# Performance work log

Hardware: AMD Instinct MI355X
Metric: run time of the kernel (lower is better)

The kernel has to match this reference:

```python
import jax, jax.numpy as jnp
import numpy as np

D2, D1, T1, T2, D3, T3 = 120, 40, 10, 5, 3, 1


def _kaiming_uniform(key, shape):
    # torch kaiming_uniform_ with nonlinearity='relu': bound = sqrt(6/fan_in), fan_in = shape[1]
    bound = np.sqrt(6.0 / shape[1])
    return jax.random.uniform(key, shape, jnp.float32, -bound, bound)


def setup_inputs() -> dict:
    key = jax.random.key(0)
    ks = jax.random.split(key, 6)
    x = jax.random.normal(ks[0], (131072, D1, T1), jnp.float32)
    return {
        "x": x,
        "BL_W1": _kaiming_uniform(ks[1], (D2, D1)),
        "BL_W2": _kaiming_uniform(ks[2], (T1, T2)),
        "BL_B": jnp.zeros((D2, T2), jnp.float32),
        "T_W1": _kaiming_uniform(ks[3], (D3, D2)),
        "T_W": jnp.full((T2, T2), 1.0 / T2, jnp.float32),
        "T_W2": _kaiming_uniform(ks[4], (T2, T3)),
        "T_B": jnp.zeros((D3, T3), jnp.float32),
        "l": jnp.full((1,), 0.5, jnp.float32),
    }


def _max_norm(w):
    # torch max_norm_: if frobenius norm > 10, rescale to norm 10 (done under no_grad)
    n = jnp.linalg.norm(w)
    scale = jnp.where(n > 10.0, 10.0 / (1e-8 + n), 1.0)
    return w * jax.lax.stop_gradient(scale)


def reference(x, BL_W1, BL_W2, BL_B, T_W1, T_W, T_W2, T_B, l):
    # --- weight clamps performed at the top of m_btabl.forward ---
    W1a = _max_norm(BL_W1)
    W2a = _max_norm(BL_W2)
    W1b = _max_norm(T_W1)
    Wb = _max_norm(T_W)
    W2b = _max_norm(T_W2)
    lam = jnp.clip(l[0], 0.0, 1.0)  # l.data clamped to [0,1]

    # BL layer: relu(W1 @ x @ W2 + B); x: [B, D1, T1] -> [B, D2, T2]
    h = jax.nn.relu(jnp.einsum('ed,bdt->bet', W1a, x) @ W2a + BL_B)
    # dropout(0.1) is identity at inference

    # TABL layer (t1 here = T2 = 5)
    X = jnp.einsum('ed,bdt->bet', W1b, h)          # [B, D3, T2]
    eye = jnp.eye(T2, dtype=jnp.float32)
    Wm = Wb - Wb * eye + eye / T2                  # force diagonal to 1/t1
    A = jax.nn.softmax(X @ Wm, axis=-1)            # temporal attention
    X = lam * X + (1.0 - lam) * X * A              # convex combination
    y = X @ W2b + T_B                              # [B, D3, 1]

    y = jnp.squeeze(y)                             # [B, D3]
    return jax.nn.softmax(y, axis=1)
```

## Files before the change

### kernel.cpp

```cpp
#include <hip/hip_runtime.h>


typedef float f32x16 __attribute__((ext_vector_type(16)));
typedef float f32x8  __attribute__((ext_vector_type(8)));
typedef float f32x4t __attribute__((ext_vector_type(4)));

#define NT 256

__device__ __forceinline__ float block_reduce_sum(float v, float* red, int tid) {
    #pragma unroll
    for (int off = 32; off > 0; off >>= 1) v += __shfl_xor(v, off, 64);
    if ((tid & 63) == 0) red[tid >> 6] = v;
    __syncthreads();
    float r = red[0] + red[1] + red[2] + red[3];
    __syncthreads();
    return r;
}

__global__ __launch_bounds__(NT)
void prep_kernel(const float* __restrict__ W1, const float* __restrict__ W2,
                 const float* __restrict__ B,  const float* __restrict__ Tw1,
                 const float* __restrict__ Tw, const float* __restrict__ Tw2,
                 const float* __restrict__ TB, const float* __restrict__ l,
                 float* __restrict__ ws)
{
    __shared__ float red[4];
    const int tid = threadIdx.x;
    float ss;
    ss = 0.f; for (int i = tid; i < 4800; i += NT) { float w = W1[i];  ss += w*w; }
    const float n1 = sqrtf(block_reduce_sum(ss, red, tid));
    ss = 0.f; for (int i = tid; i < 50;   i += NT) { float w = W2[i];  ss += w*w; }
    const float n2 = sqrtf(block_reduce_sum(ss, red, tid));
    ss = 0.f; for (int i = tid; i < 360;  i += NT) { float w = Tw1[i]; ss += w*w; }
    const float n3 = sqrtf(block_reduce_sum(ss, red, tid));
    ss = 0.f; for (int i = tid; i < 25;   i += NT) { float w = Tw[i];  ss += w*w; }
    const float n4 = sqrtf(block_reduce_sum(ss, red, tid));
    ss = 0.f; for (int i = tid; i < 5;    i += NT) { float w = Tw2[i]; ss += w*w; }
    const float n5 = sqrtf(block_reduce_sum(ss, red, tid));

    const float s1 = n1 > 10.f ? 10.f/(1e-8f+n1) : 1.f;
    const float s2 = n2 > 10.f ? 10.f/(1e-8f+n2) : 1.f;
    const float s3 = n3 > 10.f ? 10.f/(1e-8f+n3) : 1.f;
    const float s4 = n4 > 10.f ? 10.f/(1e-8f+n4) : 1.f;
    const float s5 = n5 > 10.f ? 10.f/(1e-8f+n5) : 1.f;

    for (int i = tid; i < 4800; i += NT) { int e = i/40,  d = i - e*40;  ws[e*48+d]      = W1[i]*s1; }
    for (int i = tid; i < 600;  i += NT) { int e = i/5,   t = i - e*5;   ws[e*48+40+t]   = B[i];     }
    for (int i = tid; i < 360;  i += NT) { int j = i/120, e = i - j*120; ws[e*48+45+j]   = Tw1[i]*s3;}
    for (int i = tid; i < 48;   i += NT) ws[120*48 + i] = 0.f;
    for (int i = tid; i < 52;   i += NT) ws[5824 + i] = (i < 50) ? W2[i]*s2 : 0.f;
    for (int i = tid; i < 36;   i += NT) {
        float v = 0.f;
        if (i < 25)      { int r = i/5, c = i - r*5; v = (r==c) ? 0.2f : Tw[i]*s4; }
        else if (i < 30) v = Tw2[i-25]*s5;
        else if (i < 33) v = TB[i-30];
        else if (i == 33){ float lv = l[0]; v = fminf(fmaxf(lv, 0.f), 1.f); }
        ws[5888 + i] = v;
    }
}

__device__ __forceinline__ float pair_sum(float v) {
    int o = __builtin_amdgcn_update_dpp(0, __float_as_int(v), 0xB1, 0xF, 0xF, true);
    return v + __int_as_float(o);
}

__device__ __forceinline__ float w2f(const f32x16& a, const f32x16& b,
                                     const f32x16& c, const f32x4t& d, int i) {
    return i < 16 ? a[i] : i < 32 ? b[i-16] : i < 48 ? c[i-32] : d[i-48];
}
__device__ __forceinline__ float c3f(const f32x16& a, const f32x16& b,
                                     const f32x4t& c, int i) {
    return i < 16 ? a[i] : i < 32 ? b[i-16] : c[i-32];
}

__global__ __launch_bounds__(NT, 3)
void btabl_main(const float* __restrict__ x, const float* __restrict__ ws,
                float* __restrict__ out, int nsamp)
{
    __shared__ float sRec[5808];

    const int tid = threadIdx.x;
    {
        const float4* src = (const float4*)ws;
        float4* dst = (float4*)sRec;
        for (int i = tid; i < 1452; i += NT) dst[i] = src[i];
    }
    __syncthreads();

    f32x16 wa, wb, wc; f32x4t wd;
    {
        const float* w2p = ws + 5824;
        asm volatile("s_load_dwordx16 %0, %4, 0x0\n\t"
                     "s_load_dwordx16 %1, %4, 0x40\n\t"
                     "s_load_dwordx16 %2, %4, 0x80\n\t"
                     "s_load_dwordx4  %3, %4, 0xc0\n\t"
                     "s_waitcnt lgkmcnt(0)"
                     : "=&s"(wa), "=&s"(wb), "=&s"(wc), "=&s"(wd)
                     : "s"(w2p));
    }

    const int pair = tid >> 1;
    const int p    = tid & 1;
    const int s    = blockIdx.x * 128 + pair;
    if (s >= nsamp) return;

    const float* xs = x + (size_t)s*400 + p*200;

    float Z[20][5];
    #pragma unroll
    for (int d0 = 0; d0 < 20; d0 += 2) {
        const float4* xv = (const float4*)(xs + d0*10);
        float4 f0 = xv[0], f1 = xv[1], f2 = xv[2], f3 = xv[3], f4 = xv[4];
        float v[20] = {f0.x,f0.y,f0.z,f0.w, f1.x,f1.y,f1.z,f1.w,
                       f2.x,f2.y,f2.z,f2.w, f3.x,f3.y,f3.z,f3.w,
                       f4.x,f4.y,f4.z,f4.w};
        #pragma unroll
        for (int r = 0; r < 2; r++) {
            #pragma unroll
            for (int t = 0; t < 5; t++) {
                float a = 0.f;
                #pragma unroll
                for (int k = 0; k < 10; k++)
                    a = fmaf(v[r*10+k], w2f(wa,wb,wc,wd, k*5+t), a);
                Z[d0+r][t] = a;
            }
        }
    }

    f32x8 bw;
    {
        const float* bp = ws + 40;
        asm volatile("s_load_dwordx8 %0, %1, 0x0\n\ts_waitcnt lgkmcnt(0)"
                     : "=&s"(bw) : "s"(bp));
    }
    float X3[15];
    #pragma unroll
    for (int i = 0; i < 15; i++) X3[i] = 0.f;

    for (int e = 0; e < 120; e++) {
        f32x8 bwn;
        {
            const float* bpn = ws + (e+1)*48 + 40;
            asm volatile("s_load_dwordx8 %0, %1, 0x0" : "=&s"(bwn) : "s"(bpn));
        }

        const float4* wr = (const float4*)(&sRec[e*48 + p*20]);
        float acc[5] = {0.f,0.f,0.f,0.f,0.f};
        #pragma unroll
        for (int c = 0; c < 5; c++) {
            float4 w = wr[c];
            #pragma unroll
            for (int t = 0; t < 5; t++) {
                acc[t] = fmaf(w.x, Z[c*4+0][t], acc[t]);
                acc[t] = fmaf(w.y, Z[c*4+1][t], acc[t]);
                acc[t] = fmaf(w.z, Z[c*4+2][t], acc[t]);
                acc[t] = fmaf(w.w, Z[c*4+3][t], acc[t]);
            }
        }
        #pragma unroll
        for (int t = 0; t < 5; t++) acc[t] = pair_sum(acc[t]);

        #pragma unroll
        for (int t = 0; t < 5; t++) {
            float h = fmaxf(acc[t] + bw[t], 0.f);
            X3[t]    = fmaf(bw[5], h, X3[t]);
            X3[5+t]  = fmaf(bw[6], h, X3[5+t]);
            X3[10+t] = fmaf(bw[7], h, X3[10+t]);
        }

        asm volatile("s_waitcnt lgkmcnt(0)" : "+s"(bwn));
        bw = bwn;
    }

    f32x16 ca, cb; f32x4t cc;
    {
        const float* cp = ws + 5888;
        asm volatile("s_load_dwordx16 %0, %3, 0x0\n\t"
                     "s_load_dwordx16 %1, %3, 0x40\n\t"
                     "s_load_dwordx4  %2, %3, 0x80\n\t"
                     "s_waitcnt lgkmcnt(0)"
                     : "=&s"(ca), "=&s"(cb), "=&s"(cc)
                     : "s"(cp));
    }
    const float lam  = c3f(ca, cb, cc, 33);
    const float olam = 1.f - lam;

    float y[3];
    #pragma unroll
    for (int j = 0; j < 3; j++) {
        float Sr[5];
        #pragma unroll
        for (int t = 0; t < 5; t++) {
            float a = 0.f;
            #pragma unroll
            for (int k = 0; k < 5; k++)
                a = fmaf(X3[j*5+k], c3f(ca, cb, cc, k*5+t), a);
            Sr[t] = a;
        }
        float m = Sr[0];
        #pragma unroll
        for (int t = 1; t < 5; t++) m = fmaxf(m, Sr[t]);
        float ex[5], se = 0.f;
        #pragma unroll
        for (int t = 0; t < 5; t++) { ex[t] = __expf(Sr[t]-m); se += ex[t]; }
        const float inv = 1.f/se;
        float yj = c3f(ca, cb, cc, 30+j);
        #pragma unroll
        for (int t = 0; t < 5; t++) {
            float a  = ex[t]*inv;
            float xc = X3[j*5+t]*(lam + olam*a);
            yj = fmaf(xc, c3f(ca, cb, cc, 25+t), yj);
        }
        y[j] = yj;
    }
    float m  = fmaxf(y[0], fmaxf(y[1], y[2]));
    float e0 = __expf(y[0]-m), e1 = __expf(y[1]-m), e2 = __expf(y[2]-m);
    float inv = 1.f/(e0+e1+e2);
    if (p == 0) {
        float* o = out + (size_t)s*3;
        o[0] = e0*inv; o[1] = e1*inv; o[2] = e2*inv;
    }
}

extern "C" void kernel_launch(void* const* d_in, const int* in_sizes, int n_in,
                              void* d_out, int out_size, void* d_ws, size_t ws_size,
                              hipStream_t stream) {
    const float* x   = (const float*)d_in[0];
    const float* W1  = (const float*)d_in[1];
    const float* W2  = (const float*)d_in[2];
    const float* B   = (const float*)d_in[3];
    const float* Tw1 = (const float*)d_in[4];
    const float* Tw  = (const float*)d_in[5];
    const float* Tw2 = (const float*)d_in[6];
    const float* TB  = (const float*)d_in[7];
    const float* l   = (const float*)d_in[8];
    float* out = (float*)d_out;
    float* ws  = (float*)d_ws;

    hipLaunchKernelGGL(prep_kernel, dim3(1), dim3(NT), 0, stream,
                       W1, W2, B, Tw1, Tw, Tw2, TB, l, ws);

    const int nsamp = in_sizes[0] / 400;
    const int grid  = (nsamp + 127) / 128;
    hipLaunchKernelGGL(btabl_main, dim3(grid), dim3(NT), 0, stream,
                       x, ws, out, nsamp);
}
```

Before: 410.3 us.

## Move the D1-to-D2 contraction onto bf16 MFMA with shared-memory staging

The 120x40 W1 contraction, previously done with per-thread fp32 FMAs, now runs as bf16 MFMA 16x16x32 tiles. W1 and the bias are packed into a bf16 image, and the bias is folded in through a one-hot column appended to Z. Each block handles 64 samples with 320 threads: five threads per sample compute the W2 projection and write bf16 Z into LDS, the waves run the MFMAs and reduce into X3, and one wave finishes the attention and softmax. This aims to remove the VALU-bound inner loop, but it gives up accuracy by rounding x·W2 and W1 to bf16, and it adds LDS traffic and two block barriers.

```diff
diff --git a/kernel.cpp b/kernel.cpp
--- a/kernel.cpp
+++ b/kernel.cpp
@@ -1,11 +1,17 @@
 #include <hip/hip_runtime.h>
 
 
-typedef float f32x16 __attribute__((ext_vector_type(16)));
-typedef float f32x8  __attribute__((ext_vector_type(8)));
-typedef float f32x4t __attribute__((ext_vector_type(4)));
-
-#define NT 256
+typedef short bf16x8 __attribute__((ext_vector_type(8)));
+typedef float f32x4v __attribute__((ext_vector_type(4)));
+
+#define NTP 256
+#define NTM 320
+
+__device__ __forceinline__ unsigned short f2bf(float f) {
+    unsigned int u = __float_as_uint(f);
+    u += 0x7FFFu + ((u >> 16) & 1u);
+    return (unsigned short)(u >> 16);
+}
 
 __device__ __forceinline__ float block_reduce_sum(float v, float* red, int tid) {
     #pragma unroll
@@ -17,7 +23,7 @@
     return r;
 }
 
-__global__ __launch_bounds__(NT)
+__global__ __launch_bounds__(NTP)
 void prep_kernel(const float* __restrict__ W1, const float* __restrict__ W2,
                  const float* __restrict__ B,  const float* __restrict__ Tw1,
                  const float* __restrict__ Tw, const float* __restrict__ Tw2,
@@ -27,15 +33,15 @@
     __shared__ float red[4];
     const int tid = threadIdx.x;
     float ss;
-    ss = 0.f; for (int i = tid; i < 4800; i += NT) { float w = W1[i];  ss += w*w; }
+    ss = 0.f; for (int i = tid; i < 4800; i += NTP) { float w = W1[i];  ss += w*w; }
     const float n1 = sqrtf(block_reduce_sum(ss, red, tid));
-    ss = 0.f; for (int i = tid; i < 50;   i += NT) { float w = W2[i];  ss += w*w; }
+    ss = 0.f; for (int i = tid; i < 50;   i += NTP) { float w = W2[i];  ss += w*w; }
     const float n2 = sqrtf(block_reduce_sum(ss, red, tid));
-    ss = 0.f; for (int i = tid; i < 360;  i += NT) { float w = Tw1[i]; ss += w*w; }
+    ss = 0.f; for (int i = tid; i < 360;  i += NTP) { float w = Tw1[i]; ss += w*w; }
     const float n3 = sqrtf(block_reduce_sum(ss, red, tid));
-    ss = 0.f; for (int i = tid; i < 25;   i += NT) { float w = Tw[i];  ss += w*w; }
+    ss = 0.f; for (int i = tid; i < 25;   i += NTP) { float w = Tw[i];  ss += w*w; }
     const float n4 = sqrtf(block_reduce_sum(ss, red, tid));
-    ss = 0.f; for (int i = tid; i < 5;    i += NT) { float w = Tw2[i]; ss += w*w; }
+    ss = 0.f; for (int i = tid; i < 5;    i += NTP) { float w = Tw2[i]; ss += w*w; }
     const float n5 = sqrtf(block_reduce_sum(ss, red, tid));
 
     const float s1 = n1 > 10.f ? 10.f/(1e-8f+n1) : 1.f;
@@ -44,181 +50,208 @@
     const float s4 = n4 > 10.f ? 10.f/(1e-8f+n4) : 1.f;
     const float s5 = n5 > 10.f ? 10.f/(1e-8f+n5) : 1.f;
 
-    for (int i = tid; i < 4800; i += NT) { int e = i/40,  d = i - e*40;  ws[e*48+d]      = W1[i]*s1; }
-    for (int i = tid; i < 600;  i += NT) { int e = i/5,   t = i - e*5;   ws[e*48+40+t]   = B[i];     }
-    for (int i = tid; i < 360;  i += NT) { int j = i/120, e = i - j*120; ws[e*48+45+j]   = Tw1[i]*s3;}
-    for (int i = tid; i < 48;   i += NT) ws[120*48 + i] = 0.f;
-    for (int i = tid; i < 52;   i += NT) ws[5824 + i] = (i < 50) ? W2[i]*s2 : 0.f;
-    for (int i = tid; i < 36;   i += NT) {
+    unsigned short* img = (unsigned short*)ws;
+    for (int i = tid; i < 129*48; i += NTP) {
+        const int e = i / 48, k = i - e*48;
         float v = 0.f;
-        if (i < 25)      { int r = i/5, c = i - r*5; v = (r==c) ? 0.2f : Tw[i]*s4; }
-        else if (i < 30) v = Tw2[i-25]*s5;
+        if (e < 120) {
+            if (k < 40)      v = W1[e*40 + k] * s1;
+            else if (k < 45) v = B[e*5 + (k-40)];
+        }
+        img[i] = f2bf(v);
+    }
+    for (int i = tid; i < 512; i += NTP) {
+        const int e = i >> 2, c = i & 3;
+        ws[3096 + i] = (c < 3 && e < 120) ? Tw1[c*120 + e] * s3 : 0.f;
+    }
+    for (int i = tid; i < 36; i += NTP) {
+        float v = 0.f;
+        if (i < 25)      { int r = i/5, c = i - r*5; v = (r == c) ? 0.2f : Tw[i]*s4; }
+        else if (i < 30) v = Tw2[i-25] * s5;
         else if (i < 33) v = TB[i-30];
         else if (i == 33){ float lv = l[0]; v = fminf(fmaxf(lv, 0.f), 1.f); }
-        ws[5888 + i] = v;
-    }
-}
-
-__device__ __forceinline__ float pair_sum(float v) {
-    int o = __builtin_amdgcn_update_dpp(0, __float_as_int(v), 0xB1, 0xF, 0xF, true);
-    return v + __int_as_float(o);
-}
-
-__device__ __forceinline__ float w2f(const f32x16& a, const f32x16& b,
-                                     const f32x16& c, const f32x4t& d, int i) {
-    return i < 16 ? a[i] : i < 32 ? b[i-16] : i < 48 ? c[i-32] : d[i-48];
-}
-__device__ __forceinline__ float c3f(const f32x16& a, const f32x16& b,
-                                     const f32x4t& c, int i) {
-    return i < 16 ? a[i] : i < 32 ? b[i-16] : c[i-32];
-}
-
-__global__ __launch_bounds__(NT, 3)
+        ws[3608 + i] = v;
+    }
+    for (int i = tid; i < 50; i += NTP) ws[3644 + i] = W2[i] * s2;
+}
+
+__global__ __launch_bounds__(NTM)
 void btabl_main(const float* __restrict__ x, const float* __restrict__ ws,
                 float* __restrict__ out, int nsamp)
 {
-    __shared__ float sRec[5808];
+    __align__(16) __shared__ unsigned short sW1[129*48];
+    __align__(16) __shared__ float          sWp[128*4];
+    __align__(16) __shared__ float          sC[36];
+    __align__(16) __shared__ unsigned short sZ[320*48 + 16];
+    __align__(16) __shared__ float          sX3[320*3];
 
     const int tid = threadIdx.x;
+
     {
         const float4* src = (const float4*)ws;
-        float4* dst = (float4*)sRec;
-        for (int i = tid; i < 1452; i += NT) dst[i] = src[i];
-    }
-    __syncthreads();
-
-    f32x16 wa, wb, wc; f32x4t wd;
+        float4* d1 = (float4*)sW1;
+        for (int i = tid; i < 774; i += NTM) d1[i] = src[i];
+        float4* d2 = (float4*)sWp;
+        for (int i = tid; i < 128; i += NTM) d2[i] = src[774 + i];
+        if (tid < 9) ((float4*)sC)[tid] = src[902 + tid];
+    }
+
     {
-        const float* w2p = ws + 5824;
-        asm volatile("s_load_dwordx16 %0, %4, 0x0\n\t"
-                     "s_load_dwordx16 %1, %4, 0x40\n\t"
-                     "s_load_dwordx16 %2, %4, 0x80\n\t"
-                     "s_load_dwordx4  %3, %4, 0xc0\n\t"
-                     "s_waitcnt lgkmcnt(0)"
-                     : "=&s"(wa), "=&s"(wb), "=&s"(wc), "=&s"(wd)
-                     : "s"(w2p));
-    }
-
-    const int pair = tid >> 1;
-    const int p    = tid & 1;
-    const int s    = blockIdx.x * 128 + pair;
-    if (s >= nsamp) return;
-
-    const float* xs = x + (size_t)s*400 + p*200;
-
-    float Z[20][5];
-    #pragma unroll
-    for (int d0 = 0; d0 < 20; d0 += 2) {
-        const float4* xv = (const float4*)(xs + d0*10);
-        float4 f0 = xv[0], f1 = xv[1], f2 = xv[2], f3 = xv[3], f4 = xv[4];
-        float v[20] = {f0.x,f0.y,f0.z,f0.w, f1.x,f1.y,f1.z,f1.w,
-                       f2.x,f2.y,f2.z,f2.w, f3.x,f3.y,f3.z,f3.w,
-                       f4.x,f4.y,f4.z,f4.w};
-        #pragma unroll
-        for (int r = 0; r < 2; r++) {
+        const int sLoc = tid / 5, c = tid - sLoc*5;
+        const int sGlob = blockIdx.x * 64 + sLoc;
+        const int sClamp = sGlob < nsamp ? sGlob : (nsamp - 1);
+        const float* W2p = ws + 3644;
+        const float* xs = x + (size_t)sClamp*400 + c*80;
+
+        float Zf[8][5];
+        #pragma unroll
+        for (int hh = 0; hh < 2; hh++) {
+            const float4* xv = (const float4*)(xs + hh*40);
+            float xf[40];
+            #pragma unroll
+            for (int i = 0; i < 10; i++) {
+                float4 q = xv[i];
+                xf[i*4+0] = q.x; xf[i*4+1] = q.y; xf[i*4+2] = q.z; xf[i*4+3] = q.w;
+            }
+            #pragma unroll
+            for (int r = 0; r < 4; r++) {
+                #pragma unroll
+                for (int t = 0; t < 5; t++) {
+                    float a = 0.f;
+                    #pragma unroll
+                    for (int k = 0; k < 10; k++)
+                        a = fmaf(xf[r*10+k], W2p[k*5+t], a);
+                    Zf[hh*4+r][t] = a;
+                }
+            }
+        }
+        const int colBase = 5 * sLoc;
+        #pragma unroll
+        for (int t = 0; t < 5; t++) {
+            bf16x8 zv;
+            #pragma unroll
+            for (int r = 0; r < 8; r++) zv[r] = (short)f2bf(Zf[r][t]);
+            *(bf16x8*)(sZ + (colBase + t)*48 + c*8) = zv;
+        }
+        bf16x8 oh = {0,0,0,0,0,0,0,0};
+        oh[c] = (short)0x3F80;
+        *(bf16x8*)(sZ + (colBase + c)*48 + 40) = oh;
+    }
+    __syncthreads();
+
+    const int wave = tid >> 6;
+    const int lane = tid & 63;
+    const int quad = lane >> 4;
+    const int m    = lane & 15;
+    const int colBase = wave * 64;
+
+    bf16x8 Bf[4][2];
+    const bf16x8 z8 = {0,0,0,0,0,0,0,0};
+    #pragma unroll
+    for (int nt = 0; nt < 4; nt++) {
+        const int col = colBase + nt*16 + m;
+        Bf[nt][0] = *(const bf16x8*)(sZ + col*48 + quad*8);
+        bf16x8 b1 = *(const bf16x8*)(sZ + col*48 + 32 + quad*8);
+        Bf[nt][1] = (quad >= 2) ? z8 : b1;
+    }
+
+    float X3p[4][3];
+    #pragma unroll
+    for (int nt = 0; nt < 4; nt++)
+        #pragma unroll
+        for (int j = 0; j < 3; j++) X3p[nt][j] = 0.f;
+
+    const f32x4v zacc = {0.f, 0.f, 0.f, 0.f};
+    #pragma unroll
+    for (int mt = 0; mt < 8; mt++) {
+        const unsigned short* arow = sW1 + (mt*16 + m)*48;
+        const bf16x8 A0 = *(const bf16x8*)(arow + quad*8);
+        const bf16x8 A1 = *(const bf16x8*)(arow + 32 + quad*8);
+        f32x4v wp[4];
+        #pragma unroll
+        for (int r = 0; r < 4; r++)
+            wp[r] = *(const f32x4v*)(sWp + (mt*16 + quad*4 + r)*4);
+        #pragma unroll
+        for (int nt = 0; nt < 4; nt++) {
+            f32x4v acc = __builtin_amdgcn_mfma_f32_16x16x32_bf16(A0, Bf[nt][0], zacc, 0, 0, 0);
+            acc = __builtin_amdgcn_mfma_f32_16x16x32_bf16(A1, Bf[nt][1], acc, 0, 0, 0);
+            #pragma unroll
+            for (int r = 0; r < 4; r++) {
+                const float h = fmaxf(acc[r], 0.f);
+                X3p[nt][0] = fmaf(wp[r][0], h, X3p[nt][0]);
+                X3p[nt][1] = fmaf(wp[r][1], h, X3p[nt][1]);
+                X3p[nt][2] = fmaf(wp[r][2], h, X3p[nt][2]);
+            }
+        }
+    }
+
+    #pragma unroll
+    for (int nt = 0; nt < 4; nt++) {
+        #pragma unroll
+        for (int j = 0; j < 3; j++) {
+            float v = X3p[nt][j];
+            v += __shfl_xor(v, 16, 64);
+            v += __shfl_xor(v, 32, 64);
+            X3p[nt][j] = v;
+        }
+    }
+    if (quad == 0) {
+        #pragma unroll
+        for (int nt = 0; nt < 4; nt++) {
+            const int col = colBase + nt*16 + m;
+            sX3[col*3 + 0] = X3p[nt][0];
+            sX3[col*3 + 1] = X3p[nt][1];
+            sX3[col*3 + 2] = X3p[nt][2];
+        }
+    }
+    __syncthreads();
+
+    if (tid < 64) {
+        const int sGlob = blockIdx.x * 64 + tid;
+        float X3v[3][5];
+        #pragma unroll
+        for (int t = 0; t < 5; t++)
+            #pragma unroll
+            for (int j = 0; j < 3; j++)
+                X3v[j][t] = sX3[(tid*5 + t)*3 + j];
+
+        const float lam  = sC[33];
+        const float olam = 1.f - lam;
+        float y[3];
+        #pragma unroll
+        for (int j = 0; j < 3; j++) {
+            float S[5];
             #pragma unroll
             for (int t = 0; t < 5; t++) {
                 float a = 0.f;
                 #pragma unroll
-                for (int k = 0; k < 10; k++)
-                    a = fmaf(v[r*10+k], w2f(wa,wb,wc,wd, k*5+t), a);
-                Z[d0+r][t] = a;
-            }
-        }
-    }
-
-    f32x8 bw;
-    {
-        const float* bp = ws + 40;
-        asm volatile("s_load_dwordx8 %0, %1, 0x0\n\ts_waitcnt lgkmcnt(0)"
-                     : "=&s"(bw) : "s"(bp));
-    }
-    float X3[15];
-    #pragma unroll
-    for (int i = 0; i < 15; i++) X3[i] = 0.f;
-
-    for (int e = 0; e < 120; e++) {
-        f32x8 bwn;
-        {
-            const float* bpn = ws + (e+1)*48 + 40;
-            asm volatile("s_load_dwordx8 %0, %1, 0x0" : "=&s"(bwn) : "s"(bpn));
-        }
-
-        const float4* wr = (const float4*)(&sRec[e*48 + p*20]);
-        float acc[5] = {0.f,0.f,0.f,0.f,0.f};
-        #pragma unroll
-        for (int c = 0; c < 5; c++) {
-            float4 w = wr[c];
+                for (int k = 0; k < 5; k++)
+                    a = fmaf(X3v[j][k], sC[k*5 + t], a);
+                S[t] = a;
+            }
+            float mx = S[0];
+            #pragma unroll
+            for (int t = 1; t < 5; t++) mx = fmaxf(mx, S[t]);
+            float ex[5], se = 0.f;
+            #pragma unroll
+            for (int t = 0; t < 5; t++) { ex[t] = __expf(S[t] - mx); se += ex[t]; }
+            const float inv = 1.f / se;
+            float yj = sC[30 + j];
             #pragma unroll
             for (int t = 0; t < 5; t++) {
-                acc[t] = fmaf(w.x, Z[c*4+0][t], acc[t]);
-                acc[t] = fmaf(w.y, Z[c*4+1][t], acc[t]);
-                acc[t] = fmaf(w.z, Z[c*4+2][t], acc[t]);
-                acc[t] = fmaf(w.w, Z[c*4+3][t], acc[t]);
-            }
-        }
-        #pragma unroll
-        for (int t = 0; t < 5; t++) acc[t] = pair_sum(acc[t]);
-
-        #pragma unroll
-        for (int t = 0; t < 5; t++) {
-            float h = fmaxf(acc[t] + bw[t], 0.f);
-            X3[t]    = fmaf(bw[5], h, X3[t]);
-            X3[5+t]  = fmaf(bw[6], h, X3[5+t]);
-            X3[10+t] = fmaf(bw[7], h, X3[10+t]);
-        }
-
-        asm volatile("s_waitcnt lgkmcnt(0)" : "+s"(bwn));
-        bw = bwn;
-    }
-
-    f32x16 ca, cb; f32x4t cc;
-    {
-        const float* cp = ws + 5888;
-        asm volatile("s_load_dwordx16 %0, %3, 0x0\n\t"
-                     "s_load_dwordx16 %1, %3, 0x40\n\t"
-                     "s_load_dwordx4  %2, %3, 0x80\n\t"
-                     "s_waitcnt lgkmcnt(0)"
-                     : "=&s"(ca), "=&s"(cb), "=&s"(cc)
-                     : "s"(cp));
-    }
-    const float lam  = c3f(ca, cb, cc, 33);
-    const float olam = 1.f - lam;
-
-    float y[3];
-    #pragma unroll
-    for (int j = 0; j < 3; j++) {
-        float Sr[5];
-        #pragma unroll
-        for (int t = 0; t < 5; t++) {
-            float a = 0.f;
-            #pragma unroll
-            for (int k = 0; k < 5; k++)
-                a = fmaf(X3[j*5+k], c3f(ca, cb, cc, k*5+t), a);
-            Sr[t] = a;
-        }
-        float m = Sr[0];
-        #pragma unroll
-        for (int t = 1; t < 5; t++) m = fmaxf(m, Sr[t]);
-        float ex[5], se = 0.f;
-        #pragma unroll
-        for (int t = 0; t < 5; t++) { ex[t] = __expf(Sr[t]-m); se += ex[t]; }
-        const float inv = 1.f/se;
-        float yj = c3f(ca, cb, cc, 30+j);
-        #pragma unroll
-        for (int t = 0; t < 5; t++) {
-            float a  = ex[t]*inv;
-            float xc = X3[j*5+t]*(lam + olam*a);
-            yj = fmaf(xc, c3f(ca, cb, cc, 25+t), yj);
-        }
-        y[j] = yj;
-    }
-    float m  = fmaxf(y[0], fmaxf(y[1], y[2]));
-    float e0 = __expf(y[0]-m), e1 = __expf(y[1]-m), e2 = __expf(y[2]-m);
-    float inv = 1.f/(e0+e1+e2);
-    if (p == 0) {
-        float* o = out + (size_t)s*3;
-        o[0] = e0*inv; o[1] = e1*inv; o[2] = e2*inv;
+                const float a  = ex[t] * inv;
+                const float xc = X3v[j][t] * (lam + olam * a);
+                yj = fmaf(xc, sC[25 + t], yj);
+            }
+            y[j] = yj;
+        }
+        const float mx = fmaxf(y[0], fmaxf(y[1], y[2]));
+        const float e0 = __expf(y[0]-mx), e1 = __expf(y[1]-mx), e2 = __expf(y[2]-mx);
+        const float inv = 1.f / (e0 + e1 + e2);
+        if (sGlob < nsamp) {
+            float* o = out + (size_t)sGlob*3;
+            o[0] = e0*inv; o[1] = e1*inv; o[2] = e2*inv;
+        }
     }
 }
 
@@ -237,11 +270,11 @@
     float* out = (float*)d_out;
     float* ws  = (float*)d_ws;
 
-    hipLaunchKernelGGL(prep_kernel, dim3(1), dim3(NT), 0, stream,
+    hipLaunchKernelGGL(prep_kernel, dim3(1), dim3(NTP), 0, stream,
                        W1, W2, B, Tw1, Tw, Tw2, TB, l, ws);
 
     const int nsamp = in_sizes[0] / 400;
-    const int grid  = (nsamp + 127) / 128;
-    hipLaunchKernelGGL(btabl_main, dim3(grid), dim3(NT), 0, stream,
+    const int grid  = (nsamp + 63) / 64;
+    hipLaunchKernelGGL(btabl_main, dim3(grid), dim3(NTM), 0, stream,
                        x, ws, out, nsamp);
 }
```

New measurement: 380.6 us. 7.2% less time.
